# Optimization experiments

Hardware: AMD Instinct MI355X
Metric: run time of the kernel (lower is better)

Reference implementation:

```python
import jax, jax.numpy as jnp
from jax import lax
import numpy as np

L = 8  # db4 filter length
DEC_LO = np.array([-0.010597401784997278, 0.032883011666982945, 0.030841381835986965,
                   -0.18703481171888114, -0.02798376941698385, 0.6308807679295904,
                   0.7148465705525415, 0.23037781330885523], dtype=np.float32)
DEC_HI = np.array([-0.23037781330885523, 0.7148465705525415, -0.6308807679295904,
                   -0.02798376941698385, 0.18703481171888114, 0.030841381835986965,
                   -0.032883011666982945, -0.010597401784997278], dtype=np.float32)
# analysis: correlation kernels are time-reversed decomposition filters (as in pytorch_wavelets)
AF = np.stack([DEC_LO[::-1], DEC_HI[::-1]])  # (2, L)
# synthesis: torch conv_transpose(rec_filt) == lhs-dilated correlation with flip(rec) = dec
SF = np.stack([DEC_LO, DEC_HI])              # (2, L)


def _afb1d(x, axis):
    # analysis filter bank along `axis` of (B, C, H, W); symmetric pad, stride 2
    B, C = x.shape[0], x.shape[1]
    N = x.shape[axis]
    outsize = (N + L - 1) // 2           # pywt symmetric coeff length
    p = 2 * (outsize - 1) - N + L        # total pad
    pad = [(0, 0)] * 4
    pad[axis] = (p // 2, (p + 1) // 2)
    xp = jnp.pad(x, pad, mode='symmetric')
    if axis == 2:
        kern, strides = AF.reshape(2, 1, L, 1), (2, 1)
    else:
        kern, strides = AF.reshape(2, 1, 1, L), (1, 2)
    kern = jnp.asarray(np.tile(kern, (C, 1, 1, 1)), dtype=x.dtype)  # (2C,1,kh,kw)
    return lax.conv_general_dilated(xp, kern, strides, 'VALID',
                                    dimension_numbers=('NCHW', 'OIHW', 'NCHW'),
                                    feature_group_count=C)


def dwt2d(x):
    # single-level 2D db4 DWT, symmetric mode (pytorch_wavelets DWTForward J=1)
    B, C = x.shape[0], x.shape[1]
    lohi = _afb1d(x, 3)                  # (B, 2C, H, W'); ch = c*2 + band_w
    y = _afb1d(lohi, 2)                  # (B, 4C, H', W'); ch = c*4 + band_w*2 + band_h
    y = y.reshape(B, C, 4, y.shape[-2], y.shape[-1])
    return y[:, :, 0], y[:, :, 1:]       # ll (B,C,H',W'), highs (B,C,3,H',W')


def _sfb1d(lo, hi, axis):
    # synthesis filter bank along `axis`: upsample-by-2 transposed conv, crop L-2
    C = lo.shape[1]
    if axis == 2:
        k0, k1 = SF[0].reshape(1, 1, L, 1), SF[1].reshape(1, 1, L, 1)
        dil, pad = (2, 1), [(1, 1), (0, 0)]   # lax pad = (L-1) - (L-2) = 1
    else:
        k0, k1 = SF[0].reshape(1, 1, 1, L), SF[1].reshape(1, 1, 1, L)
        dil, pad = (1, 2), [(0, 0), (1, 1)]
    k0 = jnp.asarray(np.tile(k0, (C, 1, 1, 1)), dtype=lo.dtype)
    k1 = jnp.asarray(np.tile(k1, (C, 1, 1, 1)), dtype=lo.dtype)
    conv = lambda v, k: lax.conv_general_dilated(
        v, k, (1, 1), pad, lhs_dilation=dil,
        dimension_numbers=('NCHW', 'OIHW', 'NCHW'), feature_group_count=C)
    return conv(lo, k0) + conv(hi, k1)


def idwt2d(ll, lh, hl, hh):
    lo = _sfb1d(ll, lh, 2)
    hi = _sfb1d(hl, hh, 2)
    return _sfb1d(lo, hi, 3)


def setup_inputs() -> dict:
    key = jax.random.key(0)
    ks = jax.random.split(key, 5)
    B, Cin, Cout, H, W = 16, 64, 64, 128, 128
    m = (H + L - 1) // 2                 # 67 wavelet modes per axis
    scale = 1.0 / (Cin * Cout)
    x = jax.random.normal(ks[0], (B, Cin, H, W), dtype=jnp.float32)
    ws = {f"w{i + 1}": scale * jax.random.uniform(ks[i + 1], (Cin, Cout, m, m), dtype=jnp.float32)
          for i in range(4)}
    return {"x": x, **ws}


def reference(x, w1, w2, w3, w4):
    ll, highs = dwt2d(x)
    mix = lambda v, w: jnp.einsum('bixy,ioxy->boxy', v, w)  # per-mode channel mixing
    out_ll = mix(ll, w1)
    lh = mix(highs[:, :, 0], w2)
    hl = mix(highs[:, :, 1], w3)
    hh = mix(highs[:, :, 2], w4)
    return idwt2d(out_ll, lh, hl, hh)
```

## Files before the change

kernel.cpp:

```cpp
#include <hip/hip_runtime.h>

#define BB 16
#define CC 64
#define HH 128
#define WW 128
#define MM 67
#define MODES (MM*MM)
#define MC 32
#define NCHUNK 141

typedef float f4 __attribute__((ext_vector_type(4)));

__constant__ float DEC_LO[8] = {-0.010597401784997278f, 0.032883011666982945f, 0.030841381835986965f,
                                -0.18703481171888114f, -0.02798376941698385f, 0.6308807679295904f,
                                0.7148465705525415f, 0.23037781330885523f};
__constant__ float DEC_HI[8] = {-0.23037781330885523f, 0.7148465705525415f, -0.6308807679295904f,
                                -0.02798376941698385f, 0.18703481171888114f, 0.030841381835986965f,
                                -0.032883011666982945f, -0.010597401784997278f};

__global__ __launch_bounds__(256) void dwt_w(const float* __restrict__ x, float* __restrict__ t1) {
    __shared__ float row[8][128];
    const int bc = blockIdx.x;
    const int h0 = blockIdx.y * 8;
    const int t  = threadIdx.x;
    {
        int r = t >> 5, c = (t & 31) << 2;
        const float4 v = *(const float4*)&x[((size_t)bc * HH + h0 + r) * WW + c];
        row[r][c] = v.x; row[r][c+1] = v.y; row[r][c+2] = v.z; row[r][c+3] = v.w;
    }
    __syncthreads();
    for (int oidx = t; oidx < 8 * 2 * MM; oidx += 256) {
        int wo = oidx % MM;
        int f  = (oidx / MM) & 1;
        int r  = oidx / (2 * MM);
        const float* flt = f ? DEC_HI : DEC_LO;
        float acc = 0.f;
        int base = 2 * wo - 6;
        #pragma unroll
        for (int k = 0; k < 8; ++k) {
            int i = base + k;
            i = (i < 0) ? (-i - 1) : i;
            i = (i >= WW) ? (2 * WW - 1 - i) : i;
            acc += row[r][i] * flt[7 - k];
        }
        t1[(((size_t)bc * 2 + f) * HH + h0 + r) * MM + wo] = acc;
    }
}

__global__ __launch_bounds__(256) void dwt_h(const float* __restrict__ t1, float* __restrict__ cf) {
    const int NH2 = (MM + 1) / 2;
    int idx = blockIdx.x * 256 + threadIdx.x;
    const int N = BB * CC * 2 * NH2 * MM;
    if (idx >= N) return;
    int wo = idx % MM;
    int hp = (idx / MM) % NH2;
    int fw = (idx / (MM * NH2)) % 2;
    int bc = idx / (MM * NH2 * 2);
    const float* src = t1 + ((size_t)(bc * 2 + fw) * HH) * MM + wo;
    float rv[10];
    #pragma unroll
    for (int k = 0; k < 10; ++k) {
        int i = 4 * hp - 6 + k;
        i = (i < 0) ? (-i - 1) : i;
        i = (i >= HH) ? (2 * HH - 1 - i) : i;
        rv[k] = src[(size_t)i * MM];
    }
    float lo0 = 0.f, hi0 = 0.f, lo1 = 0.f, hi1 = 0.f;
    #pragma unroll
    for (int k = 0; k < 8; ++k) {
        lo0 += rv[k]     * DEC_LO[7 - k];
        hi0 += rv[k]     * DEC_HI[7 - k];
        lo1 += rv[k + 2] * DEC_LO[7 - k];
        hi1 += rv[k + 2] * DEC_HI[7 - k];
    }
    int ho0 = 2 * hp, ho1 = 2 * hp + 1;
    size_t b0 = (size_t)(bc * 4 + fw * 2 + 0) * MM;
    size_t b1 = (size_t)(bc * 4 + fw * 2 + 1) * MM;
    cf[(b0 + ho0) * MM + wo] = lo0;
    cf[(b1 + ho0) * MM + wo] = hi0;
    if (ho1 < MM) {
        cf[(b0 + ho1) * MM + wo] = lo1;
        cf[(b1 + ho1) * MM + wo] = hi1;
    }
}

__global__ __launch_bounds__(256) void mix_k(const float* __restrict__ cf,
                                             const float* __restrict__ w1,
                                             const float* __restrict__ w2,
                                             const float* __restrict__ w3,
                                             const float* __restrict__ w4,
                                             float* __restrict__ out) {
    __shared__ float sc[BB][CC][MC];
    int flat = blockIdx.y * NCHUNK + blockIdx.x;
    {
        const int q = 564 / 8, r = 564 % 8;
        int xcd = flat & 7, j = flat >> 3;
        flat = (xcd < r ? xcd * (q + 1) : r * (q + 1) + (xcd - r) * q) + j;
    }
    const int band = flat / NCHUNK;
    const int m0   = min((flat % NCHUNK) * MC, MODES - MC);
    const int tid  = threadIdx.x;
    const float* w = (band == 0) ? w1 : (band == 1) ? w2 : (band == 2) ? w3 : w4;

    {
        const int c = tid & 7, r0 = tid >> 3;
        #pragma unroll
        for (int p = 0; p < 32; ++p) {
            int r = r0 + (p << 5);
            f4 v = *(const f4*)(cf + ((size_t)(r * 4) + band) * MODES + m0 + c * 4);
            *(f4*)&sc[r >> 6][r & 63][c * 4] = v;
        }
    }
    __syncthreads();

    const int lane = tid & 63, wv = tid >> 6;
    const int o2 = wv * 8 + (lane >> 3);
    const int mc4 = (lane & 7) * 4;
    const size_t IST = (size_t)CC * MODES;
    const float* wpl = w + (size_t)o2 * MODES + m0 + mc4;
    const float* wph = wpl + (size_t)32 * MODES;

    f4 accL[16], accH[16];
    #pragma unroll
    for (int b = 0; b < 16; ++b) { accL[b] = (f4)(0.f); accH[b] = (f4)(0.f); }

    f4 al0, al1, al2, al3, ah0, ah1, ah2, ah3;
    f4 bl0, bl1, bl2, bl3, bh0, bh1, bh2, bh3;
    al0 = *(const f4*)(wpl + 0 * IST);  ah0 = *(const f4*)(wph + 0 * IST);
    al1 = *(const f4*)(wpl + 1 * IST);  ah1 = *(const f4*)(wph + 1 * IST);
    al2 = *(const f4*)(wpl + 2 * IST);  ah2 = *(const f4*)(wph + 2 * IST);
    al3 = *(const f4*)(wpl + 3 * IST);  ah3 = *(const f4*)(wph + 3 * IST);

    #pragma unroll 1
    for (int ib = 0; ib < 64; ib += 8) {
        bl0 = *(const f4*)(wpl + (size_t)(ib + 4) * IST);  bh0 = *(const f4*)(wph + (size_t)(ib + 4) * IST);
        bl1 = *(const f4*)(wpl + (size_t)(ib + 5) * IST);  bh1 = *(const f4*)(wph + (size_t)(ib + 5) * IST);
        bl2 = *(const f4*)(wpl + (size_t)(ib + 6) * IST);  bh2 = *(const f4*)(wph + (size_t)(ib + 6) * IST);
        bl3 = *(const f4*)(wpl + (size_t)(ib + 7) * IST);  bh3 = *(const f4*)(wph + (size_t)(ib + 7) * IST);
        #pragma unroll
        for (int b = 0; b < 16; ++b) {
            f4 s = *(const f4*)&sc[b][ib + 0][mc4];
            accL[b] += s * al0;  accH[b] += s * ah0;
        }
        #pragma unroll
        for (int b = 0; b < 16; ++b) {
            f4 s = *(const f4*)&sc[b][ib + 1][mc4];
            accL[b] += s * al1;  accH[b] += s * ah1;
        }
        #pragma unroll
        for (int b = 0; b < 16; ++b) {
            f4 s = *(const f4*)&sc[b][ib + 2][mc4];
            accL[b] += s * al2;  accH[b] += s * ah2;
        }
        #pragma unroll
        for (int b = 0; b < 16; ++b) {
            f4 s = *(const f4*)&sc[b][ib + 3][mc4];
            accL[b] += s * al3;  accH[b] += s * ah3;
        }
        if (ib + 8 < 64) {
            al0 = *(const f4*)(wpl + (size_t)(ib + 8)  * IST);  ah0 = *(const f4*)(wph + (size_t)(ib + 8)  * IST);
            al1 = *(const f4*)(wpl + (size_t)(ib + 9)  * IST);  ah1 = *(const f4*)(wph + (size_t)(ib + 9)  * IST);
            al2 = *(const f4*)(wpl + (size_t)(ib + 10) * IST);  ah2 = *(const f4*)(wph + (size_t)(ib + 10) * IST);
            al3 = *(const f4*)(wpl + (size_t)(ib + 11) * IST);  ah3 = *(const f4*)(wph + (size_t)(ib + 11) * IST);
        }
        #pragma unroll
        for (int b = 0; b < 16; ++b) {
            f4 s = *(const f4*)&sc[b][ib + 4][mc4];
            accL[b] += s * bl0;  accH[b] += s * bh0;
        }
        #pragma unroll
        for (int b = 0; b < 16; ++b) {
            f4 s = *(const f4*)&sc[b][ib + 5][mc4];
            accL[b] += s * bl1;  accH[b] += s * bh1;
        }
        #pragma unroll
        for (int b = 0; b < 16; ++b) {
            f4 s = *(const f4*)&sc[b][ib + 6][mc4];
            accL[b] += s * bl2;  accH[b] += s * bh2;
        }
        #pragma unroll
        for (int b = 0; b < 16; ++b) {
            f4 s = *(const f4*)&sc[b][ib + 7][mc4];
            accL[b] += s * bl3;  accH[b] += s * bh3;
        }
    }

    #pragma unroll
    for (int b = 0; b < 16; ++b) {
        *(f4*)&out[((size_t)((b * CC + o2) * 4) + band) * MODES + m0 + mc4] = accL[b];
        *(f4*)&out[((size_t)((b * CC + o2 + 32) * 4) + band) * MODES + m0 + mc4] = accH[b];
    }
}

__global__ __launch_bounds__(256) void idwt_h(const float* __restrict__ mx, float* __restrict__ u1) {
    int idx = blockIdx.x * 256 + threadIdx.x;
    const int N = BB * CC * 2 * (HH / 2) * MM;
    if (idx >= N) return;
    int wo = idx % MM;
    int a  = (idx / MM) % (HH / 2);
    int fw = (idx / (MM * (HH / 2))) % 2;
    int bc = idx / (MM * (HH / 2) * 2);
    const float* lo = mx + ((size_t)(bc * 4 + fw * 2) * MODES) + wo;
    const float* hi = lo + MODES;
    float l[4], h4[4];
    #pragma unroll
    for (int q = 0; q < 4; ++q) {
        l[q]  = lo[(size_t)(a + q) * MM];
        h4[q] = hi[(size_t)(a + q) * MM];
    }
    float out0 = 0.f, out1 = 0.f;
    #pragma unroll
    for (int q = 0; q < 4; ++q) {
        out0 += l[q] * DEC_LO[2 * q + 1] + h4[q] * DEC_HI[2 * q + 1];
        out1 += l[q] * DEC_LO[2 * q]     + h4[q] * DEC_HI[2 * q];
    }
    size_t base = ((size_t)(bc * 2 + fw) * HH + 2 * a) * MM + wo;
    u1[base]      = out0;
    u1[base + MM] = out1;
}

__global__ __launch_bounds__(256) void idwt_w(const float* __restrict__ u1, float* __restrict__ out) {
    int idx = blockIdx.x * 256 + threadIdx.x;
    const int N = BB * CC * HH * (WW / 2);
    if (idx >= N) return;
    int a  = idx % (WW / 2);
    int h  = (idx / (WW / 2)) % HH;
    int bc = idx / ((WW / 2) * HH);
    const float* lo = u1 + (size_t)(bc * 2) * HH * MM + (size_t)h * MM;
    const float* hi = lo + (size_t)HH * MM;
    float l[4], h4[4];
    #pragma unroll
    for (int q = 0; q < 4; ++q) {
        l[q]  = lo[a + q];
        h4[q] = hi[a + q];
    }
    float out0 = 0.f, out1 = 0.f;
    #pragma unroll
    for (int q = 0; q < 4; ++q) {
        out0 += l[q] * DEC_LO[2 * q + 1] + h4[q] * DEC_HI[2 * q + 1];
        out1 += l[q] * DEC_LO[2 * q]     + h4[q] * DEC_HI[2 * q];
    }
    float2 r = make_float2(out0, out1);
    *(float2*)&out[((size_t)bc * HH + h) * WW + 2 * a] = r;
}

extern "C" void kernel_launch(void* const* d_in, const int* in_sizes, int n_in,
                              void* d_out, int out_size, void* d_ws, size_t ws_size,
                              hipStream_t stream) {
    const float* x  = (const float*)d_in[0];
    const float* w1 = (const float*)d_in[1];
    const float* w2 = (const float*)d_in[2];
    const float* w3 = (const float*)d_in[3];
    const float* w4 = (const float*)d_in[4];
    float* out = (float*)d_out;

    const size_t COEFF_FLTS = (size_t)BB * CC * 4 * MODES;
    float* buf1 = (float*)d_ws;
    float* buf2 = buf1 + COEFF_FLTS;

    {
        dim3 grid(BB * CC, HH / 8);
        dwt_w<<<grid, 256, 0, stream>>>(x, buf1);
    }
    {
        int N = BB * CC * 2 * ((MM + 1) / 2) * MM;
        dwt_h<<<(N + 255) / 256, 256, 0, stream>>>(buf1, buf2);
    }
    {
        dim3 grid(NCHUNK, 4);
        mix_k<<<grid, 256, 0, stream>>>(buf2, w1, w2, w3, w4, buf1);
    }
    {
        int N = BB * CC * 2 * (HH / 2) * MM;
        idwt_h<<<(N + 255) / 256, 256, 0, stream>>>(buf1, buf2);
    }
    {
        int N = BB * CC * HH * (WW / 2);
        idwt_w<<<(N + 255) / 256, 256, 0, stream>>>(buf2, out);
    }
}
```

Measured before the change: 241.0 us.

## Retile mode-mixing kernel to 4 batches x 8 outputs per thread

The per-thread register tile in the channel-mixing kernel changes from 16 batches x 2 output channels to 4 batches x 8 output channels. Each thread now loads 8 weight vectors per input channel and reuses each shared-memory coefficient read across 8 outputs, shifting traffic from LDS toward global weight loads. Launch bounds now declare one block per CU, and periodic __syncthreads are inserted to keep waves loosely in step for cache reuse of the weights. The risk is more global weight traffic per thread and lower occupancy.

```diff
diff --git a/kernel.cpp b/kernel.cpp
--- a/kernel.cpp
+++ b/kernel.cpp
@@ -84,12 +84,12 @@
     }
 }
 
-__global__ __launch_bounds__(256) void mix_k(const float* __restrict__ cf,
-                                             const float* __restrict__ w1,
-                                             const float* __restrict__ w2,
-                                             const float* __restrict__ w3,
-                                             const float* __restrict__ w4,
-                                             float* __restrict__ out) {
+__global__ __launch_bounds__(256, 1) void mix_k(const float* __restrict__ cf,
+                                                const float* __restrict__ w1,
+                                                const float* __restrict__ w2,
+                                                const float* __restrict__ w3,
+                                                const float* __restrict__ w4,
+                                                float* __restrict__ out) {
     __shared__ float sc[BB][CC][MC];
     int flat = blockIdx.y * NCHUNK + blockIdx.x;
     {
@@ -114,82 +114,66 @@
     __syncthreads();
 
     const int lane = tid & 63, wv = tid >> 6;
-    const int o2 = wv * 8 + (lane >> 3);
+    const int b0  = wv * 4;
+    const int os  = (lane >> 3) * 8;
     const int mc4 = (lane & 7) * 4;
     const size_t IST = (size_t)CC * MODES;
-    const float* wpl = w + (size_t)o2 * MODES + m0 + mc4;
-    const float* wph = wpl + (size_t)32 * MODES;
-
-    f4 accL[16], accH[16];
-    #pragma unroll
-    for (int b = 0; b < 16; ++b) { accL[b] = (f4)(0.f); accH[b] = (f4)(0.f); }
-
-    f4 al0, al1, al2, al3, ah0, ah1, ah2, ah3;
-    f4 bl0, bl1, bl2, bl3, bh0, bh1, bh2, bh3;
-    al0 = *(const f4*)(wpl + 0 * IST);  ah0 = *(const f4*)(wph + 0 * IST);
-    al1 = *(const f4*)(wpl + 1 * IST);  ah1 = *(const f4*)(wph + 1 * IST);
-    al2 = *(const f4*)(wpl + 2 * IST);  ah2 = *(const f4*)(wph + 2 * IST);
-    al3 = *(const f4*)(wpl + 3 * IST);  ah3 = *(const f4*)(wph + 3 * IST);
+    const float* wp = w + (size_t)os * MODES + m0 + mc4;
+
+    f4 acc[4][8];
+    #pragma unroll
+    for (int j = 0; j < 4; ++j)
+        #pragma unroll
+        for (int k = 0; k < 8; ++k) acc[j][k] = (f4)(0.f);
+
+    f4 wa[8], wb[8];
+    #pragma unroll
+    for (int k = 0; k < 8; ++k) wa[k] = *(const f4*)(wp + (size_t)k * MODES);
 
     #pragma unroll 1
-    for (int ib = 0; ib < 64; ib += 8) {
-        bl0 = *(const f4*)(wpl + (size_t)(ib + 4) * IST);  bh0 = *(const f4*)(wph + (size_t)(ib + 4) * IST);
-        bl1 = *(const f4*)(wpl + (size_t)(ib + 5) * IST);  bh1 = *(const f4*)(wph + (size_t)(ib + 5) * IST);
-        bl2 = *(const f4*)(wpl + (size_t)(ib + 6) * IST);  bh2 = *(const f4*)(wph + (size_t)(ib + 6) * IST);
-        bl3 = *(const f4*)(wpl + (size_t)(ib + 7) * IST);  bh3 = *(const f4*)(wph + (size_t)(ib + 7) * IST);
-        #pragma unroll
-        for (int b = 0; b < 16; ++b) {
-            f4 s = *(const f4*)&sc[b][ib + 0][mc4];
-            accL[b] += s * al0;  accH[b] += s * ah0;
-        }
-        #pragma unroll
-        for (int b = 0; b < 16; ++b) {
-            f4 s = *(const f4*)&sc[b][ib + 1][mc4];
-            accL[b] += s * al1;  accH[b] += s * ah1;
-        }
-        #pragma unroll
-        for (int b = 0; b < 16; ++b) {
-            f4 s = *(const f4*)&sc[b][ib + 2][mc4];
-            accL[b] += s * al2;  accH[b] += s * ah2;
-        }
-        #pragma unroll
-        for (int b = 0; b < 16; ++b) {
-            f4 s = *(const f4*)&sc[b][ib + 3][mc4];
-            accL[b] += s * al3;  accH[b] += s * ah3;
-        }
-        if (ib + 8 < 64) {
-            al0 = *(const f4*)(wpl + (size_t)(ib + 8)  * IST);  ah0 = *(const f4*)(wph + (size_t)(ib + 8)  * IST);
-            al1 = *(const f4*)(wpl + (size_t)(ib + 9)  * IST);  ah1 = *(const f4*)(wph + (size_t)(ib + 9)  * IST);
-            al2 = *(const f4*)(wpl + (size_t)(ib + 10) * IST);  ah2 = *(const f4*)(wph + (size_t)(ib + 10) * IST);
-            al3 = *(const f4*)(wpl + (size_t)(ib + 11) * IST);  ah3 = *(const f4*)(wph + (size_t)(ib + 11) * IST);
-        }
-        #pragma unroll
-        for (int b = 0; b < 16; ++b) {
-            f4 s = *(const f4*)&sc[b][ib + 4][mc4];
-            accL[b] += s * bl0;  accH[b] += s * bh0;
-        }
-        #pragma unroll
-        for (int b = 0; b < 16; ++b) {
-            f4 s = *(const f4*)&sc[b][ib + 5][mc4];
-            accL[b] += s * bl1;  accH[b] += s * bh1;
-        }
-        #pragma unroll
-        for (int b = 0; b < 16; ++b) {
-            f4 s = *(const f4*)&sc[b][ib + 6][mc4];
-            accL[b] += s * bl2;  accH[b] += s * bh2;
-        }
-        #pragma unroll
-        for (int b = 0; b < 16; ++b) {
-            f4 s = *(const f4*)&sc[b][ib + 7][mc4];
-            accL[b] += s * bl3;  accH[b] += s * bh3;
-        }
-    }
-
-    #pragma unroll
-    for (int b = 0; b < 16; ++b) {
-        *(f4*)&out[((size_t)((b * CC + o2) * 4) + band) * MODES + m0 + mc4] = accL[b];
-        *(f4*)&out[((size_t)((b * CC + o2 + 32) * 4) + band) * MODES + m0 + mc4] = accH[b];
-    }
+    for (int i = 0; i < CC; i += 2) {
+        if (i == 16 || i == 32 || i == 48) __syncthreads();
+        #pragma unroll
+        for (int k = 0; k < 8; ++k)
+            wb[k] = *(const f4*)(wp + (size_t)k * MODES + (size_t)(i + 1) * IST);
+        {
+            f4 s0 = *(const f4*)&sc[b0 + 0][i][mc4];
+            f4 s1 = *(const f4*)&sc[b0 + 1][i][mc4];
+            f4 s2 = *(const f4*)&sc[b0 + 2][i][mc4];
+            f4 s3 = *(const f4*)&sc[b0 + 3][i][mc4];
+            #pragma unroll
+            for (int k = 0; k < 8; ++k) {
+                acc[0][k] += s0 * wa[k];
+                acc[1][k] += s1 * wa[k];
+                acc[2][k] += s2 * wa[k];
+                acc[3][k] += s3 * wa[k];
+            }
+        }
+        if (i + 2 < CC) {
+            #pragma unroll
+            for (int k = 0; k < 8; ++k)
+                wa[k] = *(const f4*)(wp + (size_t)k * MODES + (size_t)(i + 2) * IST);
+        }
+        {
+            f4 s0 = *(const f4*)&sc[b0 + 0][i + 1][mc4];
+            f4 s1 = *(const f4*)&sc[b0 + 1][i + 1][mc4];
+            f4 s2 = *(const f4*)&sc[b0 + 2][i + 1][mc4];
+            f4 s3 = *(const f4*)&sc[b0 + 3][i + 1][mc4];
+            #pragma unroll
+            for (int k = 0; k < 8; ++k) {
+                acc[0][k] += s0 * wb[k];
+                acc[1][k] += s1 * wb[k];
+                acc[2][k] += s2 * wb[k];
+                acc[3][k] += s3 * wb[k];
+            }
+        }
+    }
+
+    #pragma unroll
+    for (int j = 0; j < 4; ++j)
+        #pragma unroll
+        for (int k = 0; k < 8; ++k)
+            *(f4*)&out[((size_t)(((b0 + j) * CC + os + k) * 4) + band) * MODES + m0 + mc4] = acc[j][k];
 }
 
 __global__ __launch_bounds__(256) void idwt_h(const float* __restrict__ mx, float* __restrict__ u1) {
```

Measured after the change: 291.8 us. +21.1%, slower.

## Fuse separable DWT and IDWT passes into per-image kernels via shared memory

Applied to the files above, without the earlier changes.

Merges the width and height analysis passes into one kernel per (batch,channel) image, keeping the intermediate 2x128x67 array in LDS instead of a global buffer. Does the same for the two synthesis passes. This removes two intermediate global round-trips and two launches. The cost is about 68KB of LDS per block, which limits occupancy to roughly two blocks per CU, and only 1024 blocks, each doing serial strided loops. The width pass now reads x directly from global memory with overlapping accesses.

```diff
diff --git a/kernel.cpp b/kernel.cpp
--- a/kernel.cpp
+++ b/kernel.cpp
@@ -18,69 +18,63 @@
                                 -0.02798376941698385f, 0.18703481171888114f, 0.030841381835986965f,
                                 -0.032883011666982945f, -0.010597401784997278f};
 
-__global__ __launch_bounds__(256) void dwt_w(const float* __restrict__ x, float* __restrict__ t1) {
-    __shared__ float row[8][128];
-    const int bc = blockIdx.x;
-    const int h0 = blockIdx.y * 8;
-    const int t  = threadIdx.x;
-    {
-        int r = t >> 5, c = (t & 31) << 2;
-        const float4 v = *(const float4*)&x[((size_t)bc * HH + h0 + r) * WW + c];
-        row[r][c] = v.x; row[r][c+1] = v.y; row[r][c+2] = v.z; row[r][c+3] = v.w;
-    }
-    __syncthreads();
-    for (int oidx = t; oidx < 8 * 2 * MM; oidx += 256) {
-        int wo = oidx % MM;
-        int f  = (oidx / MM) & 1;
-        int r  = oidx / (2 * MM);
-        const float* flt = f ? DEC_HI : DEC_LO;
-        float acc = 0.f;
+__global__ __launch_bounds__(256, 2) void dwt_f(const float* __restrict__ x, float* __restrict__ cf) {
+    __shared__ float st[2][HH][MM];
+    const int bc  = blockIdx.x;
+    const int tid = threadIdx.x;
+    const float* xr = x + (size_t)bc * HH * WW;
+
+    for (int p = tid; p < HH * MM; p += 256) {
+        int wo = p % MM, h = p / MM;
+        const float* row = xr + h * WW;
+        float lo = 0.f, hi = 0.f;
         int base = 2 * wo - 6;
         #pragma unroll
         for (int k = 0; k < 8; ++k) {
             int i = base + k;
             i = (i < 0) ? (-i - 1) : i;
             i = (i >= WW) ? (2 * WW - 1 - i) : i;
-            acc += row[r][i] * flt[7 - k];
-        }
-        t1[(((size_t)bc * 2 + f) * HH + h0 + r) * MM + wo] = acc;
-    }
-}
-
-__global__ __launch_bounds__(256) void dwt_h(const float* __restrict__ t1, float* __restrict__ cf) {
+            float v = row[i];
+            lo += v * DEC_LO[7 - k];
+            hi += v * DEC_HI[7 - k];
+        }
+        st[0][h][wo] = lo;
+        st[1][h][wo] = hi;
+    }
+    __syncthreads();
+
     const int NH2 = (MM + 1) / 2;
-    int idx = blockIdx.x * 256 + threadIdx.x;
-    const int N = BB * CC * 2 * NH2 * MM;
-    if (idx >= N) return;
-    int wo = idx % MM;
-    int hp = (idx / MM) % NH2;
-    int fw = (idx / (MM * NH2)) % 2;
-    int bc = idx / (MM * NH2 * 2);
-    const float* src = t1 + ((size_t)(bc * 2 + fw) * HH) * MM + wo;
-    float rv[10];
-    #pragma unroll
-    for (int k = 0; k < 10; ++k) {
-        int i = 4 * hp - 6 + k;
-        i = (i < 0) ? (-i - 1) : i;
-        i = (i >= HH) ? (2 * HH - 1 - i) : i;
-        rv[k] = src[(size_t)i * MM];
-    }
-    float lo0 = 0.f, hi0 = 0.f, lo1 = 0.f, hi1 = 0.f;
-    #pragma unroll
-    for (int k = 0; k < 8; ++k) {
-        lo0 += rv[k]     * DEC_LO[7 - k];
-        hi0 += rv[k]     * DEC_HI[7 - k];
-        lo1 += rv[k + 2] * DEC_LO[7 - k];
-        hi1 += rv[k + 2] * DEC_HI[7 - k];
-    }
-    int ho0 = 2 * hp, ho1 = 2 * hp + 1;
-    size_t b0 = (size_t)(bc * 4 + fw * 2 + 0) * MM;
-    size_t b1 = (size_t)(bc * 4 + fw * 2 + 1) * MM;
-    cf[(b0 + ho0) * MM + wo] = lo0;
-    cf[(b1 + ho0) * MM + wo] = hi0;
-    if (ho1 < MM) {
-        cf[(b0 + ho1) * MM + wo] = lo1;
-        cf[(b1 + ho1) * MM + wo] = hi1;
+    float* cfo = cf + (size_t)bc * 4 * MODES;
+    for (int q = tid; q < NH2 * MM; q += 256) {
+        int wo = q % MM, hp = q / MM;
+        int ho0 = 2 * hp, ho1 = 2 * hp + 1;
+        #pragma unroll
+        for (int fw = 0; fw < 2; ++fw) {
+            float rv[10];
+            #pragma unroll
+            for (int k = 0; k < 10; ++k) {
+                int i = 4 * hp - 6 + k;
+                i = (i < 0) ? (-i - 1) : i;
+                i = (i >= HH) ? (2 * HH - 1 - i) : i;
+                rv[k] = st[fw][i][wo];
+            }
+            float lo0 = 0.f, hi0 = 0.f, lo1 = 0.f, hi1 = 0.f;
+            #pragma unroll
+            for (int k = 0; k < 8; ++k) {
+                lo0 += rv[k]     * DEC_LO[7 - k];
+                hi0 += rv[k]     * DEC_HI[7 - k];
+                lo1 += rv[k + 2] * DEC_LO[7 - k];
+                hi1 += rv[k + 2] * DEC_HI[7 - k];
+            }
+            float* b0 = cfo + (size_t)(fw * 2 + 0) * MODES;
+            float* b1 = cfo + (size_t)(fw * 2 + 1) * MODES;
+            b0[ho0 * MM + wo] = lo0;
+            b1[ho0 * MM + wo] = hi0;
+            if (ho1 < MM) {
+                b0[ho1 * MM + wo] = lo1;
+                b1[ho1 * MM + wo] = hi1;
+            }
+        }
     }
 }
 
@@ -192,56 +186,52 @@
     }
 }
 
-__global__ __launch_bounds__(256) void idwt_h(const float* __restrict__ mx, float* __restrict__ u1) {
-    int idx = blockIdx.x * 256 + threadIdx.x;
-    const int N = BB * CC * 2 * (HH / 2) * MM;
-    if (idx >= N) return;
-    int wo = idx % MM;
-    int a  = (idx / MM) % (HH / 2);
-    int fw = (idx / (MM * (HH / 2))) % 2;
-    int bc = idx / (MM * (HH / 2) * 2);
-    const float* lo = mx + ((size_t)(bc * 4 + fw * 2) * MODES) + wo;
-    const float* hi = lo + MODES;
-    float l[4], h4[4];
-    #pragma unroll
-    for (int q = 0; q < 4; ++q) {
-        l[q]  = lo[(size_t)(a + q) * MM];
-        h4[q] = hi[(size_t)(a + q) * MM];
-    }
-    float out0 = 0.f, out1 = 0.f;
-    #pragma unroll
-    for (int q = 0; q < 4; ++q) {
-        out0 += l[q] * DEC_LO[2 * q + 1] + h4[q] * DEC_HI[2 * q + 1];
-        out1 += l[q] * DEC_LO[2 * q]     + h4[q] * DEC_HI[2 * q];
-    }
-    size_t base = ((size_t)(bc * 2 + fw) * HH + 2 * a) * MM + wo;
-    u1[base]      = out0;
-    u1[base + MM] = out1;
-}
-
-__global__ __launch_bounds__(256) void idwt_w(const float* __restrict__ u1, float* __restrict__ out) {
-    int idx = blockIdx.x * 256 + threadIdx.x;
-    const int N = BB * CC * HH * (WW / 2);
-    if (idx >= N) return;
-    int a  = idx % (WW / 2);
-    int h  = (idx / (WW / 2)) % HH;
-    int bc = idx / ((WW / 2) * HH);
-    const float* lo = u1 + (size_t)(bc * 2) * HH * MM + (size_t)h * MM;
-    const float* hi = lo + (size_t)HH * MM;
-    float l[4], h4[4];
-    #pragma unroll
-    for (int q = 0; q < 4; ++q) {
-        l[q]  = lo[a + q];
-        h4[q] = hi[a + q];
-    }
-    float out0 = 0.f, out1 = 0.f;
-    #pragma unroll
-    for (int q = 0; q < 4; ++q) {
-        out0 += l[q] * DEC_LO[2 * q + 1] + h4[q] * DEC_HI[2 * q + 1];
-        out1 += l[q] * DEC_LO[2 * q]     + h4[q] * DEC_HI[2 * q];
-    }
-    float2 r = make_float2(out0, out1);
-    *(float2*)&out[((size_t)bc * HH + h) * WW + 2 * a] = r;
+__global__ __launch_bounds__(256, 2) void idwt_f(const float* __restrict__ mx, float* __restrict__ out) {
+    __shared__ float su[2][HH][MM];
+    const int bc  = blockIdx.x;
+    const int tid = threadIdx.x;
+    const float* mxb = mx + (size_t)bc * 4 * MODES;
+
+    for (int p = tid; p < 2 * (HH / 2) * MM; p += 256) {
+        int wo = p % MM;
+        int a  = (p / MM) % (HH / 2);
+        int fw = p / (MM * (HH / 2));
+        const float* lo = mxb + (size_t)(fw * 2) * MODES + wo;
+        const float* hi = lo + MODES;
+        float l[4], h4[4];
+        #pragma unroll
+        for (int q = 0; q < 4; ++q) {
+            l[q]  = lo[(a + q) * MM];
+            h4[q] = hi[(a + q) * MM];
+        }
+        float o0 = 0.f, o1 = 0.f;
+        #pragma unroll
+        for (int q = 0; q < 4; ++q) {
+            o0 += l[q] * DEC_LO[2 * q + 1] + h4[q] * DEC_HI[2 * q + 1];
+            o1 += l[q] * DEC_LO[2 * q]     + h4[q] * DEC_HI[2 * q];
+        }
+        su[fw][2 * a][wo]     = o0;
+        su[fw][2 * a + 1][wo] = o1;
+    }
+    __syncthreads();
+
+    float* ob = out + (size_t)bc * HH * WW;
+    for (int p = tid; p < HH * (WW / 2); p += 256) {
+        int a = p & 63, h = p >> 6;
+        float l[4], h4[4];
+        #pragma unroll
+        for (int q = 0; q < 4; ++q) {
+            l[q]  = su[0][h][a + q];
+            h4[q] = su[1][h][a + q];
+        }
+        float o0 = 0.f, o1 = 0.f;
+        #pragma unroll
+        for (int q = 0; q < 4; ++q) {
+            o0 += l[q] * DEC_LO[2 * q + 1] + h4[q] * DEC_HI[2 * q + 1];
+            o1 += l[q] * DEC_LO[2 * q]     + h4[q] * DEC_HI[2 * q];
+        }
+        *(float2*)&ob[h * WW + 2 * a] = make_float2(o0, o1);
+    }
 }
 
 extern "C" void kernel_launch(void* const* d_in, const int* in_sizes, int n_in,
@@ -258,24 +248,10 @@
     float* buf1 = (float*)d_ws;
     float* buf2 = buf1 + COEFF_FLTS;
 
-    {
-        dim3 grid(BB * CC, HH / 8);
-        dwt_w<<<grid, 256, 0, stream>>>(x, buf1);
-    }
-    {
-        int N = BB * CC * 2 * ((MM + 1) / 2) * MM;
-        dwt_h<<<(N + 255) / 256, 256, 0, stream>>>(buf1, buf2);
-    }
+    dwt_f<<<BB * CC, 256, 0, stream>>>(x, buf1);
     {
         dim3 grid(NCHUNK, 4);
-        mix_k<<<grid, 256, 0, stream>>>(buf2, w1, w2, w3, w4, buf1);
-    }
-    {
-        int N = BB * CC * 2 * (HH / 2) * MM;
-        idwt_h<<<(N + 255) / 256, 256, 0, stream>>>(buf1, buf2);
-    }
-    {
-        int N = BB * CC * HH * (WW / 2);
-        idwt_w<<<(N + 255) / 256, 256, 0, stream>>>(buf2, out);
-    }
-}
+        mix_k<<<grid, 256, 0, stream>>>(buf1, w1, w2, w3, w4, buf2);
+    }
+    idwt_f<<<BB * CC, 256, 0, stream>>>(buf2, out);
+}
```

After: 233.1 us. -3.3%, faster.
